# Kernel tuning notes

Hardware: AMD Instinct MI355X
Metric: run time of the kernel (lower is better)

Reference implementation:

```python
import math
import jax, jax.numpy as jnp
import numpy as np

N_STEPS = 4
D_ENERGY = 128
FEATURE_DIM = 1024
B, N = 4, 2048


def setup_inputs() -> dict:
    key = jax.random.key(0)
    ks = jax.random.split(key, 5)
    scale = 1.0 / math.sqrt(FEATURE_DIM)
    return {
        "features": jax.random.normal(ks[0], (B, N, FEATURE_DIM), dtype=jnp.float32),
        "W_q": jax.random.normal(ks[1], (FEATURE_DIM, D_ENERGY), dtype=jnp.float32) * scale,
        "W_k": jax.random.normal(ks[2], (FEATURE_DIM, D_ENERGY), dtype=jnp.float32) * scale,
        "charge_w": jax.random.normal(ks[3], (FEATURE_DIM, 1), dtype=jnp.float32) * scale,
        "charge_b": jnp.zeros((1,), dtype=jnp.float32),
        "locality_scale": jnp.float32(1.0),
        "step_size": jnp.float32(0.5),
        "charge_decay": jnp.float32(0.3),
    }


def reference(features, W_q, W_k, charge_w, charge_b, locality_scale, step_size, charge_decay):
    Bn, Nn, _ = features.shape
    # compatibility: [B,N,N]
    Q = jnp.einsum("bnf,fe->bne", features, W_q)
    K = jnp.einsum("bnf,fe->bne", features, W_k)
    compat = jnp.einsum("bqe,bke->bqk", Q, K) / jnp.sqrt(jnp.float32(D_ENERGY))
    # locality bias: locality_scale / max(|i-j|, 1)
    pos = jnp.arange(Nn, dtype=jnp.float32)
    dist = jnp.maximum(jnp.abs(pos[None, :] - pos[:, None]), 1.0)
    locality = locality_scale / dist  # [N,N]
    # initial charge in (0,1): [B,N]
    charge = jax.nn.sigmoid(jnp.einsum("bnf,fo->bno", features, charge_w)[..., 0] + charge_b[0])
    base = compat + locality[None]  # [B,N,N], fixed across steps
    logits = base
    for _ in range(N_STEPS):
        attn = jax.nn.softmax(logits, axis=-1)
        received = attn.sum(axis=-2)  # [B,N] column sums
        charge = charge * (1.0 - charge_decay * jax.nn.sigmoid(received - 1.0))
        energy = -base * charge[..., :, None] * charge[..., None, :]
        logits = logits - step_size * energy
    return jax.nn.softmax(logits, axis=-1)
```

## Files before the change

kernel.cpp:

```cpp
#include <hip/hip_runtime.h>
#include <math.h>

namespace {
constexpr int NB = 4;
constexpr int NN = 2048;
constexpr int FD = 1024;
constexpr int DE = 128;
constexpr int BN = NB * NN;

constexpr size_t WSW_OFF   = 0;
constexpr size_t FH_OFF    = 8388608;
constexpr size_t FL_OFF    = 12582912;
constexpr size_t QKHL_OFF  = 16777216;
constexpr size_t C_OFF     = QKHL_OFF + 2097152;
}

typedef __attribute__((ext_vector_type(8))) short bf16x8;
typedef __attribute__((ext_vector_type(4))) float f32x4;
typedef __attribute__((ext_vector_type(8))) _Float16 f16x8;

__device__ __forceinline__ unsigned short bf16_hi(float x) {
    unsigned u = __float_as_uint(x);
    unsigned r = (u + 0x7fffu + ((u >> 16) & 1u)) >> 16;
    return (unsigned short)r;
}
__device__ __forceinline__ float bf16_val(unsigned short h) {
    return __uint_as_float((unsigned)h << 16);
}


__global__ __launch_bounds__(256) void prep(
        const float* __restrict__ feat, const float* __restrict__ Wq,
        const float* __restrict__ Wk, const float* __restrict__ cw,
        const float* __restrict__ cbias,
        unsigned short* __restrict__ Fh, unsigned short* __restrict__ Fl,
        unsigned short* __restrict__ Wqh, unsigned short* __restrict__ Wql,
        unsigned short* __restrict__ Wkh, unsigned short* __restrict__ Wkl,
        float* __restrict__ c0) {
    const int bid = blockIdx.x;
    const int tid = threadIdx.x;
    if (bid < 4096) {
        const int g = bid * 256 + tid;
        const int tile = g >> 6, lane = g & 63;
        const int tr = tile >> 5, fc = tile & 31;
        const int row = tr * 16 + (lane & 15);
        const int f0 = fc * 32 + (lane >> 4) * 8;
        const float* src = &feat[(size_t)row * FD + f0];
        ushort4 h0, l0, h1, l1;
        float4 a = *(const float4*)src;
        float4 b = *(const float4*)(src + 4);
        h0.x = bf16_hi(a.x); l0.x = bf16_hi(a.x - bf16_val(h0.x));
        h0.y = bf16_hi(a.y); l0.y = bf16_hi(a.y - bf16_val(h0.y));
        h0.z = bf16_hi(a.z); l0.z = bf16_hi(a.z - bf16_val(h0.z));
        h0.w = bf16_hi(a.w); l0.w = bf16_hi(a.w - bf16_val(h0.w));
        h1.x = bf16_hi(b.x); l1.x = bf16_hi(b.x - bf16_val(h1.x));
        h1.y = bf16_hi(b.y); l1.y = bf16_hi(b.y - bf16_val(h1.y));
        h1.z = bf16_hi(b.z); l1.z = bf16_hi(b.z - bf16_val(h1.z));
        h1.w = bf16_hi(b.w); l1.w = bf16_hi(b.w - bf16_val(h1.w));
        const size_t dst = (size_t)tile * 512 + lane * 8;
        *(ushort4*)&Fh[dst] = h0; *(ushort4*)&Fh[dst + 4] = h1;
        *(ushort4*)&Fl[dst] = l0; *(ushort4*)&Fl[dst + 4] = l1;
    } else if (bid < 4224) {
        const int wbid = bid - 4096;
        const int mat = wbid >> 6;
        const int g = (wbid & 63) * 256 + tid;
        const int tile = g >> 6, lane = g & 63;
        const int ec = tile >> 5, fc = tile & 31;
        const int e = ec * 16 + (lane & 15);
        const int f0 = fc * 32 + (lane >> 4) * 8;
        const float* W = mat ? Wk : Wq;
        unsigned short* Th = mat ? Wkh : Wqh;
        unsigned short* Tl = mat ? Wkl : Wql;
        unsigned short hh[8], ll[8];
        #pragma unroll
        for (int j = 0; j < 8; ++j) {
            float v = W[(size_t)(f0 + j) * DE + e];
            hh[j] = bf16_hi(v); ll[j] = bf16_hi(v - bf16_val(hh[j]));
        }
        const size_t dst = (size_t)tile * 512 + lane * 8;
        *(ushort4*)&Th[dst]     = make_ushort4(hh[0], hh[1], hh[2], hh[3]);
        *(ushort4*)&Th[dst + 4] = make_ushort4(hh[4], hh[5], hh[6], hh[7]);
        *(ushort4*)&Tl[dst]     = make_ushort4(ll[0], ll[1], ll[2], ll[3]);
        *(ushort4*)&Tl[dst + 4] = make_ushort4(ll[4], ll[5], ll[6], ll[7]);
    } else {
        const int wave = tid >> 6, lane = tid & 63;
        const int r = (bid - 4224) * 4 + wave;
        const float* fr = feat + (size_t)r * FD;
        float s = 0.f;
        #pragma unroll
        for (int k = 0; k < 16; ++k) { int f = lane + 64 * k; s += fr[f] * cw[f]; }
        for (int off = 32; off > 0; off >>= 1) s += __shfl_xor(s, off);
        if (lane == 0) {
            float x = s + cbias[0];
            c0[r] = 1.f / (1.f + __expf(-x));
        }
    }
}

__global__ __launch_bounds__(256) void qk_proj(
        const unsigned short* __restrict__ Fh, const unsigned short* __restrict__ Fl,
        const unsigned short* __restrict__ Wqh, const unsigned short* __restrict__ Wql,
        const unsigned short* __restrict__ Wkh, const unsigned short* __restrict__ Wkl,
        unsigned short* __restrict__ Qh, unsigned short* __restrict__ Ql,
        unsigned short* __restrict__ Kh, unsigned short* __restrict__ Kl) {
    __shared__ unsigned short lds[8192];
    const int tid = threadIdx.x;
    const int w = tid >> 6, lane = tid & 63;
    const int quad = lane >> 4, l16 = lane & 15;
    const int blk = blockIdx.x;
    const int mat = w >> 1, ec0 = (w & 1) * 4;
    const unsigned short* Bh = mat ? Wkh : Wqh;
    const unsigned short* Bl = mat ? Wkl : Wql;

    f32x4 acc[4];
    #pragma unroll
    for (int c = 0; c < 4; ++c) acc[c] = (f32x4){0.f, 0.f, 0.f, 0.f};

    for (int fc = 0; fc < 32; ++fc) {
        const size_t aoff = ((size_t)(blk * 32 + fc) * 64 + lane) * 8;
        bf16x8 aH = *(const bf16x8*)&Fh[aoff];
        bf16x8 aL = *(const bf16x8*)&Fl[aoff];
        #pragma unroll
        for (int ct = 0; ct < 4; ++ct) {
            const size_t boff = ((size_t)((ec0 + ct) * 32 + fc) * 64 + lane) * 8;
            bf16x8 bH = *(const bf16x8*)&Bh[boff];
            bf16x8 bL = *(const bf16x8*)&Bl[boff];
            acc[ct] = __builtin_amdgcn_mfma_f32_16x16x32_bf16(aH, bH, acc[ct], 0, 0, 0);
            acc[ct] = __builtin_amdgcn_mfma_f32_16x16x32_bf16(aH, bL, acc[ct], 0, 0, 0);
            acc[ct] = __builtin_amdgcn_mfma_f32_16x16x32_bf16(aL, bH, acc[ct], 0, 0, 0);
        }
    }
    #pragma unroll
    for (int ct = 0; ct < 4; ++ct) {
        const int e = (ec0 + ct) * 16 + l16;
        const int kc = e >> 5, q2 = (e >> 3) & 3, j2 = e & 7;
        #pragma unroll
        for (int reg = 0; reg < 4; ++reg) {
            const int rl = quad * 4 + reg;
            const float v = acc[ct][reg];
            const unsigned short h = bf16_hi(v);
            const unsigned short l = bf16_hi(v - bf16_val(h));
            const int idx = (kc * 64 + q2 * 16 + rl) * 8 + j2;
            lds[(mat * 2 + 0) * 2048 + idx] = h;
            lds[(mat * 2 + 1) * 2048 + idx] = l;
        }
    }
    __syncthreads();
    const size_t gbase = (size_t)blk * 2048;
    unsigned short* const dsts[4] = {Qh, Ql, Kh, Kl};
    #pragma unroll
    for (int ch = 0; ch < 4; ++ch) {
        const int o = ch * 2048 + tid * 8;
        unsigned short* dst = dsts[ch] + gbase + tid * 8;
        *(ushort4*)&dst[0] = *(const ushort4*)&lds[o];
        *(ushort4*)&dst[4] = *(const ushort4*)&lds[o + 4];
    }
}

__global__ __launch_bounds__(256) void base_mfma(
        const unsigned short* __restrict__ Qh, const unsigned short* __restrict__ Ql,
        const unsigned short* __restrict__ Kh, const unsigned short* __restrict__ Kl,
        const float* __restrict__ d_ls, _Float16* __restrict__ baseH) {
    const int tid = threadIdx.x;
    const int w = tid >> 6, lane = tid & 63;
    const int quad = lane >> 4, l16 = lane & 15;
    const int b = blockIdx.z;
    const int i0 = blockIdx.y * 128, j0 = blockIdx.x * 128;
    const int trA0 = (b * NN + i0) / 16 + w * 2;
    const int trB0 = (b * NN + j0) / 16;

    f32x4 acc[2][8];
    #pragma unroll
    for (int a = 0; a < 2; ++a)
        #pragma unroll
        for (int c = 0; c < 8; ++c) acc[a][c] = (f32x4){0.f, 0.f, 0.f, 0.f};

    #pragma unroll
    for (int kc = 0; kc < 4; ++kc) {
        bf16x8 aH[2], aL[2];
        #pragma unroll
        for (int rt = 0; rt < 2; ++rt) {
            const size_t off = ((size_t)((trA0 + rt) * 4 + kc) * 64 + lane) * 8;
            aH[rt] = *(const bf16x8*)&Qh[off];
            aL[rt] = *(const bf16x8*)&Ql[off];
        }
        #pragma unroll
        for (int ct = 0; ct < 8; ++ct) {
            const size_t off = ((size_t)((trB0 + ct) * 4 + kc) * 64 + lane) * 8;
            bf16x8 bH = *(const bf16x8*)&Kh[off];
            bf16x8 bL = *(const bf16x8*)&Kl[off];
            #pragma unroll
            for (int rt = 0; rt < 2; ++rt) {
                acc[rt][ct] = __builtin_amdgcn_mfma_f32_16x16x32_bf16(aH[rt], bH, acc[rt][ct], 0, 0, 0);
                acc[rt][ct] = __builtin_amdgcn_mfma_f32_16x16x32_bf16(aH[rt], bL, acc[rt][ct], 0, 0, 0);
                acc[rt][ct] = __builtin_amdgcn_mfma_f32_16x16x32_bf16(aL[rt], bH, acc[rt][ct], 0, 0, 0);
            }
        }
    }
    const float ls = d_ls[0];
    const float rs = 0.08838834764831845f;
    #pragma unroll
    for (int rt = 0; rt < 2; ++rt)
        #pragma unroll
        for (int reg = 0; reg < 4; ++reg) {
            const int i = i0 + w * 32 + rt * 16 + quad * 4 + reg;
            _Float16* brow = baseH + ((size_t)b * NN + i) * NN;
            #pragma unroll
            for (int ct = 0; ct < 8; ++ct) {
                const int j = j0 + ct * 16 + l16;
                const float dist = fmaxf(fabsf((float)(i - j)), 1.0f);
                brow[j] = (_Float16)(acc[rt][ct][reg] * rs + ls / dist);
            }
        }
}

template <int T, bool WO>
__global__ __launch_bounds__(256) void step_pass(
        const _Float16* __restrict__ base, const float* __restrict__ charge,
        const float* __restrict__ d_ss, float* __restrict__ P,
        float* __restrict__ out) {
    constexpr int CS_W = WO ? 1 : 4;
    constexpr int CS_N = WO ? 1 : NN;
    __shared__ float colsum[CS_W][CS_N];
    const int tid = threadIdx.x;
    const int w = tid >> 6, lane = tid & 63;
    const int blk = blockIdx.x;
    const int b = blk >> 8;
    const int r0 = (blk & 255) * 8;
    const float ss = d_ss[0];
    const size_t cb = (size_t)b << 11;
    const size_t ri0 = cb + r0 + w * 2;
    const float* chg1 = charge + (size_t)BN + cb;

    float ci[2][T > 0 ? T : 1];
    #pragma unroll
    for (int u = 0; u < T; ++u) {
        ci[0][u] = charge[(size_t)(u + 1) * BN + ri0] * ss;
        ci[1][u] = charge[(size_t)(u + 1) * BN + ri0 + 1] * ss;
    }

    float col_acc[32];
    if (!WO) {
        #pragma unroll
        for (int q = 0; q < 32; ++q) col_acc[q] = 0.f;
    }

    #pragma unroll
    for (int r = 0; r < 2; ++r) {
        const _Float16* row = base + (ri0 + r) * NN;
        f16x8 hv[4];
        #pragma unroll
        for (int k = 0; k < 4; ++k)
            hv[k] = *(const f16x8*)&row[k * 512 + lane * 8];
        float x[32];
        float se = 0.f;
        #pragma unroll
        for (int k = 0; k < 4; ++k) {
            const int c = k * 512 + lane * 8;
            float m[8];
            #pragma unroll
            for (int j = 0; j < 8; ++j) m[j] = 1.f;
            #pragma unroll
            for (int u = 0; u < T; ++u) {
                const float4 a0 = *(const float4*)&chg1[(size_t)u * BN + c];
                const float4 a1 = *(const float4*)&chg1[(size_t)u * BN + c + 4];
                const float cu = ci[r][u];
                m[0] += cu * a0.x; m[1] += cu * a0.y;
                m[2] += cu * a0.z; m[3] += cu * a0.w;
                m[4] += cu * a1.x; m[5] += cu * a1.y;
                m[6] += cu * a1.z; m[7] += cu * a1.w;
            }
            #pragma unroll
            for (int j = 0; j < 8; ++j) {
                const float v = __expf((float)hv[k][j] * m[j]);
                x[k * 8 + j] = v;
                se += v;
            }
        }
        #pragma unroll
        for (int off = 32; off > 0; off >>= 1) se += __shfl_xor(se, off);
        const float inv = 1.f / se;
        if (WO) {
            #pragma unroll
            for (int k = 0; k < 4; ++k) {
                const int c = k * 512 + lane * 8;
                float4 o0 = {x[k * 8 + 0] * inv, x[k * 8 + 1] * inv,
                             x[k * 8 + 2] * inv, x[k * 8 + 3] * inv};
                float4 o1 = {x[k * 8 + 4] * inv, x[k * 8 + 5] * inv,
                             x[k * 8 + 6] * inv, x[k * 8 + 7] * inv};
                *(float4*)&out[(ri0 + r) * NN + c]     = o0;
                *(float4*)&out[(ri0 + r) * NN + c + 4] = o1;
            }
        } else {
            #pragma unroll
            for (int q = 0; q < 32; ++q) col_acc[q] += x[q] * inv;
        }
    }

    if (!WO) {
        #pragma unroll
        for (int k = 0; k < 4; ++k) {
            const int c = k * 512 + lane * 8;
            *(float4*)&colsum[w][c]     = *(float4*)&col_acc[k * 8];
            *(float4*)&colsum[w][c + 4] = *(float4*)&col_acc[k * 8 + 4];
        }
        __syncthreads();
        float* prow = P + (size_t)blk * NN;
        #pragma unroll
        for (int k = 0; k < 8; ++k) {
            const int c = tid + 256 * k;
            prow[c] = colsum[0][c] + colsum[1][c] + colsum[2][c] + colsum[3][c];
        }
    }
}

__global__ __launch_bounds__(256) void charge_reduce(
        const float* __restrict__ P, const float* __restrict__ d_decay,
        const float* __restrict__ c_prev, float* __restrict__ c_next) {
    const int b = blockIdx.x >> 3;
    const int col = ((blockIdx.x & 7) << 8) + threadIdx.x;
    const float* p = P + ((size_t)b * 256) * NN + col;
    float s = 0.f;
    #pragma unroll 8
    for (int r = 0; r < 256; ++r) s += p[(size_t)r * NN];
    const int gi = (b << 11) + col;
    const float sg = 1.f / (1.f + __expf(1.f - s));
    c_next[gi] = c_prev[gi] * (1.f - d_decay[0] * sg);
}

extern "C" void kernel_launch(void* const* d_in, const int* in_sizes, int n_in,
                              void* d_out, int out_size, void* d_ws, size_t ws_size,
                              hipStream_t stream) {
    const float* feat  = (const float*)d_in[0];
    const float* Wq    = (const float*)d_in[1];
    const float* Wk    = (const float*)d_in[2];
    const float* cw    = (const float*)d_in[3];
    const float* cb    = (const float*)d_in[4];
    const float* ls    = (const float*)d_in[5];
    const float* ssp   = (const float*)d_in[6];
    const float* decay = (const float*)d_in[7];

    float* ws   = (float*)d_ws;
    unsigned short* Fh = (unsigned short*)(ws + FH_OFF);
    unsigned short* Fl = (unsigned short*)(ws + FL_OFF);
    unsigned short* qkhl = (unsigned short*)(ws + QKHL_OFF);
    unsigned short* Qh = qkhl;
    unsigned short* Ql = qkhl + (size_t)BN * DE;
    unsigned short* Kh = qkhl + (size_t)2 * BN * DE;
    unsigned short* Kl = qkhl + (size_t)3 * BN * DE;
    unsigned short* Wqh = (unsigned short*)(ws + WSW_OFF);
    unsigned short* Wql = Wqh + (size_t)DE * FD;
    unsigned short* Wkh = Wqh + (size_t)2 * DE * FD;
    unsigned short* Wkl = Wqh + (size_t)3 * DE * FD;
    float* charge = ws + C_OFF;
    _Float16* baseH = (_Float16*)(ws + WSW_OFF);
    float* P      = ws + FH_OFF;
    float* out    = (float*)d_out;

    prep<<<6272, 256, 0, stream>>>(feat, Wq, Wk, cw, cb,
                                   Fh, Fl, Wqh, Wql, Wkh, Wkl, charge);
    qk_proj<<<512, 256, 0, stream>>>(Fh, Fl, Wqh, Wql, Wkh, Wkl,
                                     Qh, Ql, Kh, Kl);
    base_mfma<<<dim3(NN / 128, NN / 128, NB), 256, 0, stream>>>(
        Qh, Ql, Kh, Kl, ls, baseH);

    step_pass<0, false><<<1024, 256, 0, stream>>>(baseH, charge, ssp, P, nullptr);
    charge_reduce<<<32, 256, 0, stream>>>(P, decay, charge, charge + (size_t)BN);
    step_pass<1, false><<<1024, 256, 0, stream>>>(baseH, charge, ssp, P, nullptr);
    charge_reduce<<<32, 256, 0, stream>>>(P, decay, charge + (size_t)BN, charge + (size_t)2 * BN);
    step_pass<2, false><<<1024, 256, 0, stream>>>(baseH, charge, ssp, P, nullptr);
    charge_reduce<<<32, 256, 0, stream>>>(P, decay, charge + (size_t)2 * BN, charge + (size_t)3 * BN);
    step_pass<3, false><<<1024, 256, 0, stream>>>(baseH, charge, ssp, P, nullptr);
    charge_reduce<<<32, 256, 0, stream>>>(P, decay, charge + (size_t)3 * BN, charge + (size_t)4 * BN);
    step_pass<4, true><<<1024, 256, 0, stream>>>(baseH, charge, ssp, nullptr, out);
}
```

Measured before the change: 320.2 us.

## Restructure step_pass so each thread owns fixed columns across block rows

Each thread now owns 8 fixed columns for all 8 rows in the block, so the column charge vectors are loaded once into registers instead of being reloaded for every row. Column partial sums stay in registers and are written straight to P, which removes the 32 KB shared-memory colsum buffer and its reduction. The row softmax sum is now combined across the 4 waves through a small shared array with a __syncthreads per row, and the next row is prefetched. In exchange the kernel takes 8 block barriers per launch and issues narrower per-thread loads.

```diff
diff --git a/kernel.cpp b/kernel.cpp
--- a/kernel.cpp
+++ b/kernel.cpp
@@ -219,9 +219,8 @@
         const _Float16* __restrict__ base, const float* __restrict__ charge,
         const float* __restrict__ d_ss, float* __restrict__ P,
         float* __restrict__ out) {
-    constexpr int CS_W = WO ? 1 : 4;
-    constexpr int CS_N = WO ? 1 : NN;
-    __shared__ float colsum[CS_W][CS_N];
+    constexpr int TS = T > 0 ? T : 1;
+    __shared__ float wsum[2][4];
     const int tid = threadIdx.x;
     const int w = tid >> 6, lane = tid & 63;
     const int blk = blockIdx.x;
@@ -229,88 +228,72 @@
     const int r0 = (blk & 255) * 8;
     const float ss = d_ss[0];
     const size_t cb = (size_t)b << 11;
-    const size_t ri0 = cb + r0 + w * 2;
-    const float* chg1 = charge + (size_t)BN + cb;
-
-    float ci[2][T > 0 ? T : 1];
+    const int c0 = tid * 8;
+
+    float cjv[TS][8];
     #pragma unroll
     for (int u = 0; u < T; ++u) {
-        ci[0][u] = charge[(size_t)(u + 1) * BN + ri0] * ss;
-        ci[1][u] = charge[(size_t)(u + 1) * BN + ri0 + 1] * ss;
-    }
-
-    float col_acc[32];
+        const float* s = &charge[(size_t)(u + 1) * BN + cb + c0];
+        const float4 a0 = *(const float4*)&s[0];
+        const float4 a1 = *(const float4*)&s[4];
+        cjv[u][0] = a0.x; cjv[u][1] = a0.y; cjv[u][2] = a0.z; cjv[u][3] = a0.w;
+        cjv[u][4] = a1.x; cjv[u][5] = a1.y; cjv[u][6] = a1.z; cjv[u][7] = a1.w;
+    }
+
+    float col_acc[8];
     if (!WO) {
         #pragma unroll
-        for (int q = 0; q < 32; ++q) col_acc[q] = 0.f;
-    }
-
-    #pragma unroll
-    for (int r = 0; r < 2; ++r) {
-        const _Float16* row = base + (ri0 + r) * NN;
-        f16x8 hv[4];
-        #pragma unroll
-        for (int k = 0; k < 4; ++k)
-            hv[k] = *(const f16x8*)&row[k * 512 + lane * 8];
-        float x[32];
-        float se = 0.f;
-        #pragma unroll
-        for (int k = 0; k < 4; ++k) {
-            const int c = k * 512 + lane * 8;
-            float m[8];
+        for (int j = 0; j < 8; ++j) col_acc[j] = 0.f;
+    }
+
+    const _Float16* bp = base + (cb + r0) * NN + c0;
+    f16x8 hv = *(const f16x8*)bp;
+
+    #pragma unroll
+    for (int r = 0; r < 8; ++r) {
+        f16x8 hvn;
+        if (r < 7) hvn = *(const f16x8*)(bp + (size_t)(r + 1) * NN);
+        const size_t ri = cb + r0 + r;
+        float ci[TS];
+        #pragma unroll
+        for (int u = 0; u < T; ++u)
+            ci[u] = charge[(size_t)(u + 1) * BN + ri] * ss;
+
+        float x[8];
+        float ps = 0.f;
+        #pragma unroll
+        for (int j = 0; j < 8; ++j) {
+            float m = 1.f;
             #pragma unroll
-            for (int j = 0; j < 8; ++j) m[j] = 1.f;
-            #pragma unroll
-            for (int u = 0; u < T; ++u) {
-                const float4 a0 = *(const float4*)&chg1[(size_t)u * BN + c];
-                const float4 a1 = *(const float4*)&chg1[(size_t)u * BN + c + 4];
-                const float cu = ci[r][u];
-                m[0] += cu * a0.x; m[1] += cu * a0.y;
-                m[2] += cu * a0.z; m[3] += cu * a0.w;
-                m[4] += cu * a1.x; m[5] += cu * a1.y;
-                m[6] += cu * a1.z; m[7] += cu * a1.w;
-            }
-            #pragma unroll
-            for (int j = 0; j < 8; ++j) {
-                const float v = __expf((float)hv[k][j] * m[j]);
-                x[k * 8 + j] = v;
-                se += v;
-            }
-        }
-        #pragma unroll
-        for (int off = 32; off > 0; off >>= 1) se += __shfl_xor(se, off);
-        const float inv = 1.f / se;
+            for (int u = 0; u < T; ++u) m += ci[u] * cjv[u][j];
+            const float v = __expf((float)hv[j] * m);
+            x[j] = v;
+            ps += v;
+        }
+        #pragma unroll
+        for (int off = 32; off > 0; off >>= 1) ps += __shfl_xor(ps, off);
+        if (lane == 0) wsum[r & 1][w] = ps;
+        __syncthreads();
+        const float inv = 1.f / (wsum[r & 1][0] + wsum[r & 1][1] +
+                                 wsum[r & 1][2] + wsum[r & 1][3]);
+
         if (WO) {
-            #pragma unroll
-            for (int k = 0; k < 4; ++k) {
-                const int c = k * 512 + lane * 8;
-                float4 o0 = {x[k * 8 + 0] * inv, x[k * 8 + 1] * inv,
-                             x[k * 8 + 2] * inv, x[k * 8 + 3] * inv};
-                float4 o1 = {x[k * 8 + 4] * inv, x[k * 8 + 5] * inv,
-                             x[k * 8 + 6] * inv, x[k * 8 + 7] * inv};
-                *(float4*)&out[(ri0 + r) * NN + c]     = o0;
-                *(float4*)&out[(ri0 + r) * NN + c + 4] = o1;
-            }
+            float4 o0 = {x[0] * inv, x[1] * inv, x[2] * inv, x[3] * inv};
+            float4 o1 = {x[4] * inv, x[5] * inv, x[6] * inv, x[7] * inv};
+            float* op = &out[ri * NN + c0];
+            *(float4*)&op[0] = o0;
+            *(float4*)&op[4] = o1;
         } else {
             #pragma unroll
-            for (int q = 0; q < 32; ++q) col_acc[q] += x[q] * inv;
-        }
+            for (int j = 0; j < 8; ++j) col_acc[j] += x[j] * inv;
+        }
+        hv = hvn;
     }
 
     if (!WO) {
-        #pragma unroll
-        for (int k = 0; k < 4; ++k) {
-            const int c = k * 512 + lane * 8;
-            *(float4*)&colsum[w][c]     = *(float4*)&col_acc[k * 8];
-            *(float4*)&colsum[w][c + 4] = *(float4*)&col_acc[k * 8 + 4];
-        }
-        __syncthreads();
-        float* prow = P + (size_t)blk * NN;
-        #pragma unroll
-        for (int k = 0; k < 8; ++k) {
-            const int c = tid + 256 * k;
-            prow[c] = colsum[0][c] + colsum[1][c] + colsum[2][c] + colsum[3][c];
-        }
+        float* prow = P + (size_t)blk * NN + c0;
+        *(float4*)&prow[0] = *(float4*)&col_acc[0];
+        *(float4*)&prow[4] = *(float4*)&col_acc[4];
     }
 }
 
```

Result: faster. 282.0 us (-11.9%).
